# Performance work log

Hardware: AMD Instinct MI355X
Metric: run time of the kernel (lower is better)

The kernel has to match this reference:

```python
import jax, jax.numpy as jnp
import numpy as np

N = 50000      # nodes
E = 800000     # edges
C_IN = 128
C_HID = 128
C_OUT = 128
LN_EPS = 1e-5  # PyG LayerNorm default eps


def setup_inputs() -> dict:
    key = jax.random.key(0)
    ks = jax.random.split(key, 8)
    x = jax.random.normal(ks[0], (N, C_IN), jnp.float32)
    edge_index = jax.random.randint(ks[1], (2, E), 0, N, dtype=jnp.int32)
    s1 = 1.0 / np.sqrt(C_IN)
    s2 = 1.0 / np.sqrt(C_HID)
    return {
        "x": x,
        "edge_index": edge_index,
        "eps1": jnp.float32(1e-4),              # GINConv train_eps init
        "W1": jax.random.normal(ks[2], (C_HID, C_IN), jnp.float32) * s1,
        "b1": jnp.zeros((C_HID,), jnp.float32),
        "ln_w": jnp.ones((C_HID,), jnp.float32),
        "ln_b": jnp.zeros((C_HID,), jnp.float32),
        "prelu_a": jnp.float32(0.25),           # nn.PReLU default single param
        "eps2": jnp.float32(1e-4),
        "W2": jax.random.normal(ks[3], (C_OUT, C_HID), jnp.float32) * s2,
        "b2": jnp.zeros((C_OUT,), jnp.float32),
    }


def _gin_max(x, src, dst, eps, W, b):
    # GINConv(aggr='max'): nn((1+eps)*x + max_{j in N(i)} x_j)
    msg = x[src]                                          # [E, C] gather
    agg = jax.ops.segment_max(msg, dst, num_segments=N)   # [N, C]
    agg = jnp.where(jnp.isfinite(agg), agg, jnp.float32(0.0))  # empty segments -> 0 (PyG fill)
    h = (1.0 + eps) * x + agg
    return h @ W.T + b


def _graph_layernorm(x, w, b):
    # PyG LayerNorm mode='graph', single graph: normalize over ALL nodes & channels
    x = x - jnp.mean(x)
    x = x / (jnp.std(x) + LN_EPS)
    return x * w + b


def reference(x, edge_index, eps1, W1, b1, ln_w, ln_b, prelu_a, eps2, W2, b2):
    src, dst = edge_index[0], edge_index[1]
    h = _gin_max(x, src, dst, eps1, W1, b1)
    h = _graph_layernorm(h, ln_w, ln_b)
    h = jnp.where(h >= 0, h, prelu_a * h)  # PReLU
    return _gin_max(h, src, dst, eps2, W2, b2)
```

## Files before the change

### kernel.cpp

```cpp
#include <hip/hip_runtime.h>
#include <hip/hip_fp16.h>
#include <math.h>

#define NN 50000
#define NE 800000
#define C  128
#define BKT 128
#define NBUK ((NN + BKT - 1) / BKT)
#define ECHUNK 2048
#define NEBLK ((NE + ECHUNK - 1) / ECHUNK)
#define SAP 136

typedef _Float16 f16x8 __attribute__((ext_vector_type(8)));
typedef float f32x4 __attribute__((ext_vector_type(4)));

__global__ void k_wh(const float* __restrict__ W1, const float* __restrict__ W2,
                     _Float16* __restrict__ Wh1, _Float16* __restrict__ Wh2) {
  int i = blockIdx.x * 256 + threadIdx.x;
  if (i < C * C) Wh1[i] = (_Float16)W1[i];
  else if (i < 2 * C * C) Wh2[i - C * C] = (_Float16)W2[i - C * C];
}

__global__ __launch_bounds__(256) void k_bh(const int* __restrict__ dst,
                                            int* __restrict__ bh) {
  __shared__ int h[NBUK];
  int t = threadIdx.x;
  for (int i = t; i < NBUK; i += 256) h[i] = 0;
  __syncthreads();
  int base = blockIdx.x * ECHUNK;
  int end = base + ECHUNK; if (end > NE) end = NE;
  for (int e = base + t; e < end; e += 256) atomicAdd(&h[dst[e] >> 7], 1);
  __syncthreads();
  for (int i = t; i < NBUK; i += 256) bh[i * NEBLK + blockIdx.x] = h[i];
}

__global__ __launch_bounds__(256) void k_bscan(int* __restrict__ bh,
                                               int* __restrict__ btot) {
  int b = blockIdx.x, t = threadIdx.x;
  int lane = t & 63, wid = t >> 6;
  __shared__ int wsum[4];
  int carry = 0;
  for (int base = 0; base < NEBLK; base += 256) {
    int i = base + t;
    int v = (i < NEBLK) ? bh[b * NEBLK + i] : 0;
    int incl = v;
    #pragma unroll
    for (int off = 1; off < 64; off <<= 1) {
      int u = __shfl_up(incl, off, 64);
      if (lane >= off) incl += u;
    }
    if (lane == 63) wsum[wid] = incl;
    __syncthreads();
    int woff = 0;
    #pragma unroll
    for (int wI = 0; wI < 4; ++wI) if (wI < wid) woff += wsum[wI];
    if (i < NEBLK) bh[b * NEBLK + i] = carry + woff + incl - v;
    int total = wsum[0] + wsum[1] + wsum[2] + wsum[3];
    __syncthreads();
    carry += total;
  }
  if (t == 0) btot[b] = carry;
}

__global__ __launch_bounds__(256) void k_bbase(const int* __restrict__ btot,
                                               int* __restrict__ bbase,
                                               int* __restrict__ rowstart) {
  int t = threadIdx.x;
  int lane = t & 63, wid = t >> 6;
  __shared__ int wsum[4];
  int carry = 0;
  for (int base = 0; base < NBUK; base += 256) {
    int i = base + t;
    int v = (i < NBUK) ? btot[i] : 0;
    int incl = v;
    #pragma unroll
    for (int off = 1; off < 64; off <<= 1) {
      int u = __shfl_up(incl, off, 64);
      if (lane >= off) incl += u;
    }
    if (lane == 63) wsum[wid] = incl;
    __syncthreads();
    int woff = 0;
    #pragma unroll
    for (int wI = 0; wI < 4; ++wI) if (wI < wid) woff += wsum[wI];
    if (i < NBUK) bbase[i] = carry + woff + incl - v;
    int total = wsum[0] + wsum[1] + wsum[2] + wsum[3];
    __syncthreads();
    carry += total;
  }
  if (t == 0) rowstart[NN] = NE;
}

__global__ __launch_bounds__(256) void k_bscatter(const int* __restrict__ src,
                       const int* __restrict__ dst,
                       const int* __restrict__ bh, const int* __restrict__ bbase,
                       int2* __restrict__ binned) {
  __shared__ int cur[NBUK];
  int t = threadIdx.x, blk = blockIdx.x;
  for (int i = t; i < NBUK; i += 256) cur[i] = bbase[i] + bh[i * NEBLK + blk];
  __syncthreads();
  int base = blk * ECHUNK;
  int end = base + ECHUNK; if (end > NE) end = NE;
  for (int e = base + t; e < end; e += 256) {
    int d = dst[e];
    int pos = atomicAdd(&cur[d >> 7], 1);
    binned[pos] = make_int2(src[e], d);
  }
}

__global__ __launch_bounds__(256) void k_bfill(const int2* __restrict__ binned,
                       const int* __restrict__ bbase, const int* __restrict__ btot,
                       int* __restrict__ rowstart, int* __restrict__ csr) {
  int b = blockIdx.x, t = threadIdx.x;
  __shared__ int hist[BKT];
  __shared__ int cur[BKT];
  __shared__ int wsum[4];
  int s0 = bbase[b];
  int cnt = btot[b];
  if (t < BKT) hist[t] = 0;
  __syncthreads();
  for (int j = t; j < cnt; j += 256) atomicAdd(&hist[binned[s0 + j].y & (BKT - 1)], 1);
  __syncthreads();
  int v = (t < BKT) ? hist[t] : 0;
  int lane = t & 63, wid = t >> 6;
  int incl = v;
  #pragma unroll
  for (int off = 1; off < 64; off <<= 1) {
    int u = __shfl_up(incl, off, 64);
    if (lane >= off) incl += u;
  }
  if (lane == 63) wsum[wid] = incl;
  __syncthreads();
  int woff = 0;
  #pragma unroll
  for (int wI = 0; wI < 4; ++wI) if (wI < wid) woff += wsum[wI];
  int excl = woff + incl - v;
  if (t < BKT) {
    cur[t] = excl;
    int node = b * BKT + t;
    if (node < NN) rowstart[node] = s0 + excl;
  }
  __syncthreads();
  for (int j = t; j < cnt; j += 256) {
    int2 sd = binned[s0 + j];
    int p = atomicAdd(&cur[sd.y & (BKT - 1)], 1);
    csr[s0 + p] = sd.x;
  }
}

__global__ __launch_bounds__(256) void k_tohalf(const float* __restrict__ in,
                                                __half2* __restrict__ o) {
  int i = blockIdx.x * 256 + threadIdx.x;
  if (i < NN * C / 4) {
    float4 v = ((const float4*)in)[i];
    o[2 * i]     = __floats2half2_rn(v.x, v.y);
    o[2 * i + 1] = __floats2half2_rn(v.z, v.w);
  }
}

template<int MODE>
__global__ __launch_bounds__(256) void k_agg_gemm(const __half2* __restrict__ xh2,
                       const int* __restrict__ rs, const int* __restrict__ csr,
                       const float* __restrict__ eps_p,
                       const _Float16* __restrict__ Wh, const float* __restrict__ bias,
                       _Float16* __restrict__ outh, float* __restrict__ outf,
                       double* __restrict__ st) {
  __shared__ _Float16 sA[16 * SAP];
  int t = threadIdx.x, wid = t >> 6, lane = t & 63;
  int nbase = blockIdx.x * 16;
  float e1v = 1.0f + eps_p[0];

  #pragma unroll
  for (int k = 0; k < 4; ++k) {
    int nl = wid * 4 + k;
    int n = nbase + nl;
    int s0 = rs[n], s1 = rs[n + 1];
    float a0 = -INFINITY, a1 = -INFINITY, b0 = -INFINITY, b1 = -INFINITY;
    float c0 = -INFINITY, c1 = -INFINITY, d0 = -INFINITY, d1 = -INFINITY;
    int j = s0;
    for (; j + 3 < s1; j += 4) {
      int e0 = csr[j], e1_ = csr[j + 1], e2 = csr[j + 2], e3 = csr[j + 3];
      __half2 v0 = xh2[(size_t)e0 * 64 + lane];
      __half2 v1 = xh2[(size_t)e1_ * 64 + lane];
      __half2 v2 = xh2[(size_t)e2 * 64 + lane];
      __half2 v3 = xh2[(size_t)e3 * 64 + lane];
      a0 = fmaxf(a0, __low2float(v0)); a1 = fmaxf(a1, __high2float(v0));
      b0 = fmaxf(b0, __low2float(v1)); b1 = fmaxf(b1, __high2float(v1));
      c0 = fmaxf(c0, __low2float(v2)); c1 = fmaxf(c1, __high2float(v2));
      d0 = fmaxf(d0, __low2float(v3)); d1 = fmaxf(d1, __high2float(v3));
    }
    for (; j < s1; ++j) {
      int e0 = csr[j];
      __half2 v0 = xh2[(size_t)e0 * 64 + lane];
      a0 = fmaxf(a0, __low2float(v0)); a1 = fmaxf(a1, __high2float(v0));
    }
    float m0 = fmaxf(fmaxf(a0, b0), fmaxf(c0, d0));
    float m1 = fmaxf(fmaxf(a1, b1), fmaxf(c1, d1));
    if (s1 == s0) { m0 = 0.f; m1 = 0.f; }
    __half2 xs = xh2[(size_t)n * 64 + lane];
    float ox = fmaf(e1v, __low2float(xs), m0);
    float oy = fmaf(e1v, __high2float(xs), m1);
    ((__half2*)(sA + nl * SAP))[lane] = __floats2half2_rn(ox, oy);
  }
  __syncthreads();

  int r = lane & 15, kq = lane >> 4;
  const _Float16* arow = sA + r * SAP + kq * 8;
  f32x4 acc[2];
  #pragma unroll
  for (int oi = 0; oi < 2; ++oi) {
    float bv = bias[(wid * 2 + oi) * 16 + r];
    f32x4 z = {bv, bv, bv, bv};
    acc[oi] = z;
  }
  #pragma unroll
  for (int kk = 0; kk < 4; ++kk) {
    f16x8 a = *(const f16x8*)(arow + kk * 32);
    #pragma unroll
    for (int oi = 0; oi < 2; ++oi) {
      int ot = wid * 2 + oi;
      f16x8 b = *(const f16x8*)(Wh + ((size_t)ot * 16 + r) * C + kk * 32 + kq * 8);
      acc[oi] = __builtin_amdgcn_mfma_f32_16x16x32_f16(a, b, acc[oi], 0, 0, 0);
    }
  }

  float s = 0.f, ss = 0.f;
  #pragma unroll
  for (int oi = 0; oi < 2; ++oi) {
    int ot = wid * 2 + oi;
    #pragma unroll
    for (int j = 0; j < 4; ++j) {
      float v = acc[oi][j];
      size_t off = (size_t)(nbase + kq * 4 + j) * C + ot * 16 + r;
      if (MODE == 0) {
        outh[off] = (_Float16)v;
        s += v; ss += v * v;
      } else {
        __builtin_nontemporal_store(v, &outf[off]);
      }
    }
  }
  if (MODE == 0) {
    #pragma unroll
    for (int off = 32; off > 0; off >>= 1) {
      s  += __shfl_down(s, off, 64);
      ss += __shfl_down(ss, off, 64);
    }
    __shared__ float sdl[4], ssl[4];
    if (lane == 0) { sdl[wid] = s; ssl[wid] = ss; }
    __syncthreads();
    if (t == 0) {
      atomicAdd(&st[0], (double)(sdl[0] + sdl[1] + sdl[2] + sdl[3]));
      atomicAdd(&st[1], (double)(ssl[0] + ssl[1] + ssl[2] + ssl[3]));
    }
  }
}

__global__ void k_final(const double* __restrict__ st, float* __restrict__ scal) {
  double M = (double)NN * C;
  double mean = st[0] / M;
  double var = st[1] / M - mean * mean;
  if (var < 0.0) var = 0.0;
  double stdv = sqrt(var);
  scal[0] = (float)mean;
  scal[1] = (float)(1.0 / (stdv + 1e-5));
}

__global__ __launch_bounds__(256) void k_act_h(const _Float16* __restrict__ h,
                       const float* __restrict__ scal,
                       const float* __restrict__ lw, const float* __restrict__ lb,
                       const float* __restrict__ a_p, _Float16* __restrict__ outh) {
  int i = blockIdx.x * 256 + threadIdx.x;
  if (i >= NN * C / 8) return;
  float mean = scal[0], inv = scal[1], a = a_p[0];
  f16x8 v = ((const f16x8*)h)[i];
  int c8 = i & 15;
  float4 w0 = ((const float4*)lw)[c8 * 2], w1 = ((const float4*)lw)[c8 * 2 + 1];
  float4 b0 = ((const float4*)lb)[c8 * 2], b1 = ((const float4*)lb)[c8 * 2 + 1];
  float wv[8] = {w0.x, w0.y, w0.z, w0.w, w1.x, w1.y, w1.z, w1.w};
  float bv[8] = {b0.x, b0.y, b0.z, b0.w, b1.x, b1.y, b1.z, b1.w};
  f16x8 res;
  #pragma unroll
  for (int k = 0; k < 8; ++k) {
    float r = ((float)v[k] - mean) * inv * wv[k] + bv[k];
    r = (r >= 0.f) ? r : a * r;
    res[k] = (_Float16)r;
  }
  ((f16x8*)outh)[i] = res;
}

extern "C" void kernel_launch(void* const* d_in, const int* in_sizes, int n_in,
                              void* d_out, int out_size, void* d_ws, size_t ws_size,
                              hipStream_t stream) {
  const float* x    = (const float*)d_in[0];
  const int*   ei   = (const int*)d_in[1];
  const float* eps1 = (const float*)d_in[2];
  const float* W1   = (const float*)d_in[3];
  const float* b1   = (const float*)d_in[4];
  const float* lnw  = (const float*)d_in[5];
  const float* lnb  = (const float*)d_in[6];
  const float* pa   = (const float*)d_in[7];
  const float* eps2 = (const float*)d_in[8];
  const float* W2   = (const float*)d_in[9];
  const float* b2   = (const float*)d_in[10];
  float* out = (float*)d_out;
  const int* srcI = ei;
  const int* dstI = ei + NE;

  char* w = (char*)d_ws;
  _Float16* Bh     = (_Float16*)(w);
  __half2*  xh     = (__half2*)(w + 12800000);
  _Float16* Wh1    = (_Float16*)(w + 25600000);
  _Float16* Wh2    = (_Float16*)(w + 25632768);
  int*      rowst  = (int*)(w + 25665536);
  int*      csr    = (int*)(w + 25865600);
  int2*     binned = (int2*)(w + 29065600);
  int*      bh     = (int*)(w + 35465600);
  int*      btot   = (int*)(w + 36077184);
  int*      bbase  = (int*)(w + 36078848);
  double*   st     = (double*)(w + 36080512);
  float*    scal   = (float*)(w + 36080528);

  hipMemsetAsync(st, 0, 2 * sizeof(double), stream);

  k_wh<<<128, 256, 0, stream>>>(W1, W2, Wh1, Wh2);

  k_bh<<<NEBLK, 256, 0, stream>>>(dstI, bh);
  k_bscan<<<NBUK, 256, 0, stream>>>(bh, btot);
  k_bbase<<<1, 256, 0, stream>>>(btot, bbase, rowst);
  k_bscatter<<<NEBLK, 256, 0, stream>>>(srcI, dstI, bh, bbase, binned);
  k_bfill<<<NBUK, 256, 0, stream>>>(binned, bbase, btot, rowst, csr);

  k_tohalf<<<(NN * C / 4 + 255) / 256, 256, 0, stream>>>(x, xh);

  k_agg_gemm<0><<<NN / 16, 256, 0, stream>>>(xh, rowst, csr, eps1, Wh1, b1,
                                             Bh, nullptr, st);

  k_final<<<1, 1, 0, stream>>>(st, scal);
  k_act_h<<<(NN * C / 8 + 255) / 256, 256, 0, stream>>>(Bh, scal, lnw, lnb, pa,
                                                        (_Float16*)xh);

  k_agg_gemm<1><<<NN / 16, 256, 0, stream>>>(xh, rowst, csr, eps2, Wh2, b2,
                                             nullptr, out, nullptr);
}
```

Before: 293.3 us.

## Split fused aggregate+GEMM into separate gather and MFMA GEMM kernels

Unfuses the max-aggregation from the MFMA GEMM. One kernel now handles one node per wave with an 8-way unrolled gather and writes a half-precision pre-activation buffer. A separate GEMM kernel then has each wave compute a full 16x128 output tile. The aim is higher gather parallelism and more memory-level parallelism per wave, with the GEMM stage free of the serialized per-block aggregation. The cost is an extra round trip of a 12.8MB intermediate through global memory and two more kernel launches.

```diff
diff --git a/kernel.cpp b/kernel.cpp
--- a/kernel.cpp
+++ b/kernel.cpp
@@ -9,7 +9,6 @@
 #define NBUK ((NN + BKT - 1) / BKT)
 #define ECHUNK 2048
 #define NEBLK ((NE + ECHUNK - 1) / ECHUNK)
-#define SAP 136
 
 typedef _Float16 f16x8 __attribute__((ext_vector_type(8)));
 typedef float f32x4 __attribute__((ext_vector_type(4)));
@@ -158,85 +157,106 @@
   }
 }
 
+__global__ __launch_bounds__(256) void k_agg_h(const __half2* __restrict__ xh2,
+                       const int* __restrict__ rs, const int* __restrict__ csr,
+                       const float* __restrict__ eps_p, __half2* __restrict__ preh2) {
+  int wid = threadIdx.x >> 6;
+  int lane = threadIdx.x & 63;
+  int n = blockIdx.x * 4 + wid;
+  if (n >= NN) return;
+  int s0 = rs[n], s1 = rs[n + 1];
+  float a0 = -INFINITY, a1 = -INFINITY, b0 = -INFINITY, b1 = -INFINITY;
+  float c0 = -INFINITY, c1 = -INFINITY, d0 = -INFINITY, d1 = -INFINITY;
+  float e0a = -INFINITY, e1a = -INFINITY, f0 = -INFINITY, f1 = -INFINITY;
+  float g0 = -INFINITY, g1 = -INFINITY, h0 = -INFINITY, h1 = -INFINITY;
+  int j = s0;
+  for (; j + 7 < s1; j += 8) {
+    int i0 = csr[j], i1 = csr[j + 1], i2 = csr[j + 2], i3 = csr[j + 3];
+    int i4 = csr[j + 4], i5 = csr[j + 5], i6 = csr[j + 6], i7 = csr[j + 7];
+    __half2 v0 = xh2[(size_t)i0 * 64 + lane];
+    __half2 v1 = xh2[(size_t)i1 * 64 + lane];
+    __half2 v2 = xh2[(size_t)i2 * 64 + lane];
+    __half2 v3 = xh2[(size_t)i3 * 64 + lane];
+    __half2 v4 = xh2[(size_t)i4 * 64 + lane];
+    __half2 v5 = xh2[(size_t)i5 * 64 + lane];
+    __half2 v6 = xh2[(size_t)i6 * 64 + lane];
+    __half2 v7 = xh2[(size_t)i7 * 64 + lane];
+    a0 = fmaxf(a0, __low2float(v0));  a1 = fmaxf(a1, __high2float(v0));
+    b0 = fmaxf(b0, __low2float(v1));  b1 = fmaxf(b1, __high2float(v1));
+    c0 = fmaxf(c0, __low2float(v2));  c1 = fmaxf(c1, __high2float(v2));
+    d0 = fmaxf(d0, __low2float(v3));  d1 = fmaxf(d1, __high2float(v3));
+    e0a = fmaxf(e0a, __low2float(v4)); e1a = fmaxf(e1a, __high2float(v4));
+    f0 = fmaxf(f0, __low2float(v5));  f1 = fmaxf(f1, __high2float(v5));
+    g0 = fmaxf(g0, __low2float(v6));  g1 = fmaxf(g1, __high2float(v6));
+    h0 = fmaxf(h0, __low2float(v7));  h1 = fmaxf(h1, __high2float(v7));
+  }
+  for (; j + 3 < s1; j += 4) {
+    int i0 = csr[j], i1 = csr[j + 1], i2 = csr[j + 2], i3 = csr[j + 3];
+    __half2 v0 = xh2[(size_t)i0 * 64 + lane];
+    __half2 v1 = xh2[(size_t)i1 * 64 + lane];
+    __half2 v2 = xh2[(size_t)i2 * 64 + lane];
+    __half2 v3 = xh2[(size_t)i3 * 64 + lane];
+    a0 = fmaxf(a0, __low2float(v0)); a1 = fmaxf(a1, __high2float(v0));
+    b0 = fmaxf(b0, __low2float(v1)); b1 = fmaxf(b1, __high2float(v1));
+    c0 = fmaxf(c0, __low2float(v2)); c1 = fmaxf(c1, __high2float(v2));
+    d0 = fmaxf(d0, __low2float(v3)); d1 = fmaxf(d1, __high2float(v3));
+  }
+  for (; j < s1; ++j) {
+    int i0 = csr[j];
+    __half2 v0 = xh2[(size_t)i0 * 64 + lane];
+    a0 = fmaxf(a0, __low2float(v0)); a1 = fmaxf(a1, __high2float(v0));
+  }
+  float m0 = fmaxf(fmaxf(fmaxf(a0, b0), fmaxf(c0, d0)), fmaxf(fmaxf(e0a, f0), fmaxf(g0, h0)));
+  float m1 = fmaxf(fmaxf(fmaxf(a1, b1), fmaxf(c1, d1)), fmaxf(fmaxf(e1a, f1), fmaxf(g1, h1)));
+  if (s1 == s0) { m0 = 0.f; m1 = 0.f; }
+  float e1v = 1.0f + eps_p[0];
+  __half2 xs = xh2[(size_t)n * 64 + lane];
+  float ox = fmaf(e1v, __low2float(xs), m0);
+  float oy = fmaf(e1v, __high2float(xs), m1);
+  preh2[(size_t)n * 64 + lane] = __floats2half2_rn(ox, oy);
+}
+
 template<int MODE>
-__global__ __launch_bounds__(256) void k_agg_gemm(const __half2* __restrict__ xh2,
-                       const int* __restrict__ rs, const int* __restrict__ csr,
-                       const float* __restrict__ eps_p,
+__global__ __launch_bounds__(256) void k_gemm_f16(const _Float16* __restrict__ Ah,
                        const _Float16* __restrict__ Wh, const float* __restrict__ bias,
                        _Float16* __restrict__ outh, float* __restrict__ outf,
                        double* __restrict__ st) {
-  __shared__ _Float16 sA[16 * SAP];
-  int t = threadIdx.x, wid = t >> 6, lane = t & 63;
-  int nbase = blockIdx.x * 16;
-  float e1v = 1.0f + eps_p[0];
-
-  #pragma unroll
-  for (int k = 0; k < 4; ++k) {
-    int nl = wid * 4 + k;
-    int n = nbase + nl;
-    int s0 = rs[n], s1 = rs[n + 1];
-    float a0 = -INFINITY, a1 = -INFINITY, b0 = -INFINITY, b1 = -INFINITY;
-    float c0 = -INFINITY, c1 = -INFINITY, d0 = -INFINITY, d1 = -INFINITY;
-    int j = s0;
-    for (; j + 3 < s1; j += 4) {
-      int e0 = csr[j], e1_ = csr[j + 1], e2 = csr[j + 2], e3 = csr[j + 3];
-      __half2 v0 = xh2[(size_t)e0 * 64 + lane];
-      __half2 v1 = xh2[(size_t)e1_ * 64 + lane];
-      __half2 v2 = xh2[(size_t)e2 * 64 + lane];
-      __half2 v3 = xh2[(size_t)e3 * 64 + lane];
-      a0 = fmaxf(a0, __low2float(v0)); a1 = fmaxf(a1, __high2float(v0));
-      b0 = fmaxf(b0, __low2float(v1)); b1 = fmaxf(b1, __high2float(v1));
-      c0 = fmaxf(c0, __low2float(v2)); c1 = fmaxf(c1, __high2float(v2));
-      d0 = fmaxf(d0, __low2float(v3)); d1 = fmaxf(d1, __high2float(v3));
-    }
-    for (; j < s1; ++j) {
-      int e0 = csr[j];
-      __half2 v0 = xh2[(size_t)e0 * 64 + lane];
-      a0 = fmaxf(a0, __low2float(v0)); a1 = fmaxf(a1, __high2float(v0));
-    }
-    float m0 = fmaxf(fmaxf(a0, b0), fmaxf(c0, d0));
-    float m1 = fmaxf(fmaxf(a1, b1), fmaxf(c1, d1));
-    if (s1 == s0) { m0 = 0.f; m1 = 0.f; }
-    __half2 xs = xh2[(size_t)n * 64 + lane];
-    float ox = fmaf(e1v, __low2float(xs), m0);
-    float oy = fmaf(e1v, __high2float(xs), m1);
-    ((__half2*)(sA + nl * SAP))[lane] = __floats2half2_rn(ox, oy);
-  }
-  __syncthreads();
-
-  int r = lane & 15, kq = lane >> 4;
-  const _Float16* arow = sA + r * SAP + kq * 8;
-  f32x4 acc[2];
-  #pragma unroll
-  for (int oi = 0; oi < 2; ++oi) {
-    float bv = bias[(wid * 2 + oi) * 16 + r];
-    f32x4 z = {bv, bv, bv, bv};
-    acc[oi] = z;
-  }
-  #pragma unroll
-  for (int kk = 0; kk < 4; ++kk) {
-    f16x8 a = *(const f16x8*)(arow + kk * 32);
-    #pragma unroll
-    for (int oi = 0; oi < 2; ++oi) {
-      int ot = wid * 2 + oi;
-      f16x8 b = *(const f16x8*)(Wh + ((size_t)ot * 16 + r) * C + kk * 32 + kq * 8);
-      acc[oi] = __builtin_amdgcn_mfma_f32_16x16x32_f16(a, b, acc[oi], 0, 0, 0);
-    }
-  }
-
+  int wid = threadIdx.x >> 6, lane = threadIdx.x & 63;
+  int nt = blockIdx.x * 4 + wid;
+  int r = lane & 15;
+  int kq = lane >> 4;
   float s = 0.f, ss = 0.f;
-  #pragma unroll
-  for (int oi = 0; oi < 2; ++oi) {
-    int ot = wid * 2 + oi;
-    #pragma unroll
-    for (int j = 0; j < 4; ++j) {
-      float v = acc[oi][j];
-      size_t off = (size_t)(nbase + kq * 4 + j) * C + ot * 16 + r;
-      if (MODE == 0) {
-        outh[off] = (_Float16)v;
-        s += v; ss += v * v;
-      } else {
-        __builtin_nontemporal_store(v, &outf[off]);
+  if (nt < NN / 16) {
+    const _Float16* arow = Ah + ((size_t)nt * 16 + r) * C + kq * 8;
+    f32x4 acc[8];
+    #pragma unroll
+    for (int ot = 0; ot < 8; ++ot) {
+      float bv = bias[ot * 16 + r];
+      f32x4 z = {bv, bv, bv, bv};
+      acc[ot] = z;
+    }
+    #pragma unroll
+    for (int kk = 0; kk < 4; ++kk) {
+      f16x8 a = *(const f16x8*)(arow + kk * 32);
+      #pragma unroll
+      for (int ot = 0; ot < 8; ++ot) {
+        f16x8 b = *(const f16x8*)(Wh + ((size_t)ot * 16 + r) * C + kk * 32 + kq * 8);
+        acc[ot] = __builtin_amdgcn_mfma_f32_16x16x32_f16(a, b, acc[ot], 0, 0, 0);
+      }
+    }
+    size_t nbase = (size_t)nt * 16;
+    #pragma unroll
+    for (int ot = 0; ot < 8; ++ot) {
+      #pragma unroll
+      for (int j = 0; j < 4; ++j) {
+        float v = acc[ot][j];
+        size_t off = (nbase + kq * 4 + j) * C + ot * 16 + r;
+        if (MODE == 0) {
+          outh[off] = (_Float16)v;
+          s += v; ss += v * v;
+        } else {
+          __builtin_nontemporal_store(v, &outf[off]);
+        }
       }
     }
   }
@@ -249,7 +269,7 @@
     __shared__ float sdl[4], ssl[4];
     if (lane == 0) { sdl[wid] = s; ssl[wid] = ss; }
     __syncthreads();
-    if (t == 0) {
+    if (threadIdx.x == 0) {
       atomicAdd(&st[0], (double)(sdl[0] + sdl[1] + sdl[2] + sdl[3]));
       atomicAdd(&st[1], (double)(ssl[0] + ssl[1] + ssl[2] + ssl[3]));
     }
@@ -310,16 +330,17 @@
   char* w = (char*)d_ws;
   _Float16* Bh     = (_Float16*)(w);
   __half2*  xh     = (__half2*)(w + 12800000);
-  _Float16* Wh1    = (_Float16*)(w + 25600000);
-  _Float16* Wh2    = (_Float16*)(w + 25632768);
-  int*      rowst  = (int*)(w + 25665536);
-  int*      csr    = (int*)(w + 25865600);
-  int2*     binned = (int2*)(w + 29065600);
-  int*      bh     = (int*)(w + 35465600);
-  int*      btot   = (int*)(w + 36077184);
-  int*      bbase  = (int*)(w + 36078848);
-  double*   st     = (double*)(w + 36080512);
-  float*    scal   = (float*)(w + 36080528);
+  __half2*  preh   = (__half2*)(w + 25600000);
+  _Float16* Wh1    = (_Float16*)(w + 38400000);
+  _Float16* Wh2    = (_Float16*)(w + 38432768);
+  int*      rowst  = (int*)(w + 38465536);
+  int*      csr    = (int*)(w + 38665600);
+  int2*     binned = (int2*)(w + 41865600);
+  int*      bh     = (int*)(w + 48265600);
+  int*      btot   = (int*)(w + 48877184);
+  int*      bbase  = (int*)(w + 48878848);
+  double*   st     = (double*)(w + 48880512);
+  float*    scal   = (float*)(w + 48880528);
 
   hipMemsetAsync(st, 0, 2 * sizeof(double), stream);
 
@@ -333,13 +354,15 @@
 
   k_tohalf<<<(NN * C / 4 + 255) / 256, 256, 0, stream>>>(x, xh);
 
-  k_agg_gemm<0><<<NN / 16, 256, 0, stream>>>(xh, rowst, csr, eps1, Wh1, b1,
-                                             Bh, nullptr, st);
+  k_agg_h<<<(NN + 3) / 4, 256, 0, stream>>>(xh, rowst, csr, eps1, preh);
+  k_gemm_f16<0><<<(NN / 16 + 3) / 4, 256, 0, stream>>>((const _Float16*)preh, Wh1, b1,
+                                                       Bh, nullptr, st);
 
   k_final<<<1, 1, 0, stream>>>(st, scal);
   k_act_h<<<(NN * C / 8 + 255) / 256, 256, 0, stream>>>(Bh, scal, lnw, lnb, pa,
                                                         (_Float16*)xh);
 
-  k_agg_gemm<1><<<NN / 16, 256, 0, stream>>>(xh, rowst, csr, eps2, Wh2, b2,
-                                             nullptr, out, nullptr);
-}
+  k_agg_h<<<(NN + 3) / 4, 256, 0, stream>>>(xh, rowst, csr, eps2, preh);
+  k_gemm_f16<1><<<(NN / 16 + 3) / 4, 256, 0, stream>>>((const _Float16*)preh, Wh2, b2,
+                                                       nullptr, out, nullptr);
+}
```

After: 258.6 us. -11.9%, faster.
